# Kernel tuning notes

Hardware: AMD Instinct MI355X
Metric: run time of the kernel (lower is better)

## Reference

```python
import jax, jax.numpy as jnp
import numpy as np

B, N, D, H = 64, 257, 1024, 16
HD = D // H  # 64


def setup_inputs() -> dict:
    key = jax.random.key(0)
    k1, k2, k3, k4, k5, k6 = jax.random.split(key, 6)
    x = jax.random.normal(k1, (B, N, D), dtype=jnp.float32)
    # boolean key mask per batch; never mask CLS token (col 0) so no fully-masked rows
    mask = jax.random.randint(k2, (B, N), 0, 2) > 0
    mask = mask.at[:, 0].set(False)
    s = 1.0 / np.sqrt(D)
    in_proj_w = jax.random.normal(k3, (3 * D, D), dtype=jnp.float32) * s
    in_proj_b = jax.random.normal(k4, (3 * D,), dtype=jnp.float32) * 0.02
    out_proj_w = jax.random.normal(k5, (D, D), dtype=jnp.float32) * s
    out_proj_b = jax.random.normal(k6, (D,), dtype=jnp.float32) * 0.02
    return {"x": x, "mask": mask, "in_proj_w": in_proj_w, "in_proj_b": in_proj_b,
            "out_proj_w": out_proj_w, "out_proj_b": out_proj_b}


def reference(x, mask, in_proj_w, in_proj_b, out_proj_w, out_proj_b):
    b, n, d = x.shape
    h, hd = H, d // H
    # fused QKV projection: [b, n, 3*d]
    qkv = jnp.einsum('bnd,ed->bne', x, in_proj_w) + in_proj_b
    # einops 'b n (qkv h d) -> qkv b h n d'
    qkv = qkv.reshape(b, n, 3, h, hd).transpose(2, 0, 3, 1, 4)
    q, k, v = qkv[0], qkv[1], qkv[2]  # each [b, h, n, hd]
    attn_weights = jnp.einsum('bhqe,bhke->bhqk', q, k) / jnp.sqrt(jnp.asarray(hd, x.dtype))
    # mode == 'mask': -inf on masked keys (broadcast over heads and queries)
    attn_weights = jnp.where(mask[:, None, None, :], -jnp.inf, attn_weights)
    attn_matrix = jax.nn.softmax(attn_weights, axis=-1)
    out = jnp.einsum('bhqk,bhke->bhqe', attn_matrix, v)  # [b, h, n, hd]
    out = out.transpose(0, 2, 1, 3).reshape(b, n, d)      # 'b h n d -> b n (h d)'
    return jnp.einsum('bnd,ed->bne', out, out_proj_w) + out_proj_b
```

## Files before the change

### kernel.cpp

```cpp
#include <hip/hip_runtime.h>

#define B_   64
#define N_   257
#define D_   1024
#define H_   16
#define HD_  64
#define M_   (B_*N_)
#define CK_  96
#define VTS_ 128
#define PLS_ 104

typedef __bf16 bf16x8 __attribute__((ext_vector_type(8)));
typedef __bf16 bf16x4 __attribute__((ext_vector_type(4)));
typedef float  f32x4  __attribute__((ext_vector_type(4)));

__device__ __forceinline__ void gload_lds16(const void* g, void* l) {
    __builtin_amdgcn_global_load_lds(
        (const __attribute__((address_space(1))) void*)g,
        (__attribute__((address_space(3))) void*)l, 16, 0, 0);
}

#define MEMF() asm volatile("" ::: "memory")
#define BARRIER() do { MEMF(); __builtin_amdgcn_s_barrier(); MEMF(); } while (0)
#define WAITV(n) asm volatile("s_waitcnt vmcnt(" #n ")" ::: "memory")

#define XQ_  4210688
#define W1Q_ 786432
#define W2Q_ 262144
__global__ __launch_bounds__(256) void cvt_all(const float* __restrict__ x,
                                               const float* __restrict__ w1,
                                               const float* __restrict__ w2,
                                               __bf16* __restrict__ xb,
                                               __bf16* __restrict__ w1b,
                                               __bf16* __restrict__ w2b) {
    int i = blockIdx.x * 256 + threadIdx.x;
    const float* src; __bf16* dst; int j;
    if (i < XQ_) { src = x; dst = xb; j = i; }
    else if (i < XQ_ + W1Q_) { src = w1; dst = w1b; j = i - XQ_; }
    else if (i < XQ_ + W1Q_ + W2Q_) { src = w2; dst = w2b; j = i - XQ_ - W1Q_; }
    else return;
    float4 v = reinterpret_cast<const float4*>(src)[j];
    bf16x4 o;
    o[0] = (__bf16)v.x; o[1] = (__bf16)v.y; o[2] = (__bf16)v.z; o[3] = (__bf16)v.w;
    *reinterpret_cast<bf16x4*>(dst + (size_t)j * 4) = o;
}

template<int NT, int MODE>
__global__ __launch_bounds__(512, 2) void gemm256(const __bf16* __restrict__ A,
                                                  const __bf16* __restrict__ W,
                                                  const float* __restrict__ bias,
                                                  __bf16* __restrict__ qo,
                                                  __bf16* __restrict__ ko,
                                                  __bf16* __restrict__ vo,
                                                  float* __restrict__ fo) {
    __shared__ __align__(16) char smem[131072];
    constexpr int NWG = 65 * NT;
    constexpr int qd = NWG >> 3, rm = NWG & 7;
    const int orig = blockIdx.x;
    const int xcd = orig & 7, loc = orig >> 3;
    const int wgid = (xcd < rm ? xcd * (qd + 1) : rm * (qd + 1) + (xcd - rm) * qd) + loc;
    const int rowt = wgid / NT, colt = wgid - rowt * NT;
    const int row0 = rowt * 256, col0 = colt * 256;

    const int tid = threadIdx.x, lane = tid & 63, wv = tid >> 6;
    const int wm = wv >> 2, wn = wv & 3;
    const int fr = lane & 15, fq = lane >> 4, frs = lane & 7;

    const int pr = tid >> 3;
    const int pg = ((tid & 7) ^ (pr & 7)) * 8;
    int srcA[4];
    {
        const int prow[4] = {0, 128, 64, 192};
#pragma unroll
        for (int p = 0; p < 4; ++p) {
            int rg = row0 + prow[p] + pr;
            if (rg > M_ - 1) rg = M_ - 1;
            srcA[p] = rg * 1024 + pg;
        }
    }
    int srcW[2], ldsW[2];
#pragma unroll
    for (int e = 0; e < 2; ++e) {
        const int wb = (wv >> 1) * 64 + e * 16 + (wv & 1) * 8;
        srcW[e] = (col0 + wb + (lane >> 3)) * 1024 + pg;
        ldsW[e] = wb * 128;
    }
    char* const At0 = smem;
    char* const At1 = smem + 32768;
    char* const Wt0 = smem + 65536;
    char* const Wt1 = smem + 98304;

#define STG_AF(dst, kk) do { gload_lds16(A + srcA[0] + (kk), (dst) + wv * 1024); \
                             gload_lds16(A + srcA[1] + (kk), (dst) + 16384 + wv * 1024); } while (0)
#define STG_AB(dst, kk) do { gload_lds16(A + srcA[2] + (kk), (dst) + 8192 + wv * 1024); \
                             gload_lds16(A + srcA[3] + (kk), (dst) + 24576 + wv * 1024); } while (0)
#define STG_WF(dst, kk) do { gload_lds16(W + srcW[0] + (kk), (dst) + ldsW[0]); \
                             gload_lds16(W + srcW[1] + (kk), (dst) + ldsW[1]); } while (0)
#define STG_WB(dst, kk) do { gload_lds16(W + srcW[0] + 32768 + (kk), (dst) + ldsW[0] + 4096); \
                             gload_lds16(W + srcW[1] + 32768 + (kk), (dst) + ldsW[1] + 4096); } while (0)
#define LD_A(buf, rqo) do { \
    _Pragma("unroll") for (int i = 0; i < 4; ++i) \
    _Pragma("unroll") for (int ks = 0; ks < 2; ++ks) \
        af[i][ks] = *(const bf16x8*)((buf) + (wm * 128 + (rqo) + i * 16 + fr) * 128 \
                                           + (((ks * 4 + fq) ^ frs) << 4)); \
} while (0)
#define LD_B(buf, co, bw) do { \
    _Pragma("unroll") for (int j = 0; j < 2; ++j) \
    _Pragma("unroll") for (int ks = 0; ks < 2; ++ks) \
        bw[j][ks] = *(const bf16x8*)((buf) + (wn * 64 + (co) + j * 16 + fr) * 128 \
                                           + (((ks * 4 + fq) ^ frs) << 4)); \
} while (0)
#define MFMA_Q(i0, j0, bw) do { \
    __builtin_amdgcn_s_setprio(1); \
    _Pragma("unroll") for (int i = 0; i < 4; ++i) \
    _Pragma("unroll") for (int j = 0; j < 2; ++j) \
    _Pragma("unroll") for (int ks = 0; ks < 2; ++ks) \
        acc[(i0) + i][(j0) + j] = __builtin_amdgcn_mfma_f32_16x16x32_bf16( \
            af[i][ks], bw[j][ks], acc[(i0) + i][(j0) + j], 0, 0, 0); \
    __builtin_amdgcn_s_setprio(0); \
} while (0)

    f32x4 acc[8][4] = {};
    bf16x8 af[4][2], bw0[2][2], bw1[2][2];

    STG_AF(At0, 0); STG_WF(Wt0, 0); STG_WB(Wt0, 0); STG_AB(At0, 0);
    WAITV(4);
    BARRIER();

#pragma unroll 2
    for (int t = 0; t < 16; ++t) {
        char* const Ac = (t & 1) ? At1 : At0;
        char* const Wc = (t & 1) ? Wt1 : Wt0;
        char* const An = (t & 1) ? At0 : At1;
        char* const Wn = (t & 1) ? Wt0 : Wt1;
        const int kk = (t < 15) ? (t + 1) * 64 : 960;
        LD_A(Ac, 0);
        LD_B(Wc, 0, bw0);
        STG_AF(An, kk);
        WAITV(4);
        BARRIER();
        MFMA_Q(0, 0, bw0);
        BARRIER();
        LD_B(Wc, 32, bw1);
        STG_WF(Wn, kk);
        WAITV(4);
        BARRIER();
        MFMA_Q(0, 2, bw1);
        BARRIER();
        LD_A(Ac, 64);
        STG_WB(Wn, kk);
        BARRIER();
        MFMA_Q(4, 2, bw1);
        BARRIER();
        STG_AB(An, kk);
        WAITV(4);
        BARRIER();
        MFMA_Q(4, 0, bw0);
        BARRIER();
    }
    WAITV(0);
    BARRIER();

    if constexpr (MODE == 0) {
        const int which = colt >> 2;
        __bf16* const dst = which == 0 ? qo : (which == 1 ? ko : vo);
        const float scale = which == 0 ? 0.125f : 1.0f;
        float bj[4];
#pragma unroll
        for (int j = 0; j < 4; ++j) bj[j] = bias[col0 + wn * 64 + j * 16 + fr];
        __bf16* const Ct = (__bf16*)smem;
#pragma unroll
        for (int i = 0; i < 8; ++i) {
            const int rb = wm * 128 + (i >> 2) * 64 + (i & 3) * 16 + fq * 4;
#pragma unroll
            for (int r = 0; r < 4; ++r) {
                const int row = rb + r;
#pragma unroll
                for (int j = 0; j < 4; ++j) {
                    const int cu = wn * 64 + j * 16 + fr;
                    Ct[row * 256 + (((cu >> 3) ^ (row & 7)) * 8) + (cu & 7)] =
                        (__bf16)((acc[i][j][r] + bj[j]) * scale);
                }
            }
        }
        BARRIER();
#pragma unroll
        for (int p = 0; p < 16; ++p) {
            const int row = p * 16 + (tid >> 5);
            const int m = row0 + row;
            if (m < M_) {
                const int gl = tid & 31;
                bf16x8 v = *(const bf16x8*)(Ct + row * 256 + ((gl ^ (row & 7)) * 8));
                const int cG = col0 + gl * 8;
                const int h = (cG >> 6) & 15, hd = cG & 63;
                const int bb = m / 257, nn = m - bb * 257;
                *reinterpret_cast<bf16x8*>(dst + ((size_t)(bb * 16 + h) * 257 + nn) * 64 + hd) = v;
            }
        }
    } else {
        float bj[4];
#pragma unroll
        for (int j = 0; j < 4; ++j) bj[j] = bias[col0 + wn * 64 + j * 16 + fr];
#pragma unroll
        for (int i = 0; i < 8; ++i) {
            const int rb = wm * 128 + (i >> 2) * 64 + (i & 3) * 16 + fq * 4;
#pragma unroll
            for (int r = 0; r < 4; ++r) {
                const int m = row0 + rb + r;
                if (m < M_) {
                    float* const p = fo + (size_t)m * 1024 + col0 + wn * 64 + fr;
#pragma unroll
                    for (int j = 0; j < 4; ++j) p[j * 16] = acc[i][j][r] + bj[j];
                }
            }
        }
    }
#undef STG_AF
#undef STG_AB
#undef STG_WF
#undef STG_WB
#undef LD_A
#undef LD_B
#undef MFMA_Q
}

__global__ __launch_bounds__(256) void attn_kernel(const __bf16* __restrict__ qw,
                                                   const __bf16* __restrict__ kw,
                                                   const __bf16* __restrict__ vw,
                                                   const int* __restrict__ mask,
                                                   __bf16* __restrict__ attn) {
    const int bh = blockIdx.x;
    const int bb = bh >> 4, hh = bh & 15;
    const int q0 = blockIdx.y * 64;
    const int tid = threadIdx.x, lane = tid & 63, wv = tid >> 6;
    const int fr = lane & 15, fq = lane >> 4;
    const float NEG_INF = -__builtin_inff();

    __shared__ __align__(16) __bf16 Qs[64 * 64];
    __shared__ __align__(16) __bf16 Ks[CK_ * 64];
    __shared__ __align__(16) __bf16 Vt[64 * VTS_];
    __shared__ __align__(16) __bf16 Pl[4][16 * PLS_];
    __shared__ float maskb[288];

    const __bf16* qg = qw + ((size_t)bh * 257 + q0) * 64;
    const __bf16* kg = kw + (size_t)bh * 257 * 64;
    const __bf16* vg = vw + (size_t)bh * 257 * 64;
    const int* mg = mask + bb * 257;

    for (int idx = tid; idx < 288; idx += 256)
        maskb[idx] = (idx < 257 && mg[idx] == 0) ? 0.0f : NEG_INF;

#pragma unroll
    for (int i = 0; i < 2; ++i) {
        const int c = tid + i * 256;
        const int r = c >> 3, g = (c & 7) ^ (r & 7);
        gload_lds16(qg + (size_t)r * 64 + g * 8, (char*)Qs + i * 4096 + wv * 1024);
    }

    float m_run[4] = {NEG_INF, NEG_INF, NEG_INF, NEG_INF};
    float l_run[4] = {};
    f32x4 Oa[4] = {};

    for (int c3 = 0; c3 < 3; ++c3) {
        const int k0 = c3 * CK_;
        __syncthreads();
#pragma unroll
        for (int i = 0; i < 3; ++i) {
            const int c = tid + i * 256;
            const int r = c >> 3, g = (c & 7) ^ (r & 7);
            if (k0 + r < 257)
                gload_lds16(kg + (size_t)(k0 + r) * 64 + g * 8, (char*)Ks + i * 4096 + wv * 1024);
        }
#pragma unroll
        for (int it = 0; it < 3; ++it) {
            const int t = tid + it * 256;
            const int key = t >> 3, grp = t & 7;
            if (k0 + key < 257) {
                bf16x8 v8 = *reinterpret_cast<const bf16x8*>(vg + (size_t)(k0 + key) * 64 + grp * 8);
#pragma unroll
                for (int u = 0; u < 8; ++u) {
                    const int hd = grp * 8 + u;
                    Vt[hd * VTS_ + (((key >> 3) ^ (hd & 7)) * 8) + (key & 7)] = v8[u];
                }
            }
        }
        __syncthreads();

        f32x4 s[6];
        {
            bf16x8 aq[2];
#pragma unroll
            for (int ks = 0; ks < 2; ++ks)
                aq[ks] = *reinterpret_cast<const bf16x8*>(
                    &Qs[(wv * 16 + fr) * 64 + (((ks * 4 + fq) ^ (fr & 7)) * 8)]);
#pragma unroll
            for (int nt = 0; nt < 6; ++nt) {
                f32x4 sa = {};
#pragma unroll
                for (int ks = 0; ks < 2; ++ks) {
                    bf16x8 bk = *reinterpret_cast<const bf16x8*>(
                        &Ks[(nt * 16 + fr) * 64 + (((ks * 4 + fq) ^ (fr & 7)) * 8)]);
                    sa = __builtin_amdgcn_mfma_f32_16x16x32_bf16(aq[ks], bk, sa, 0, 0, 0);
                }
                const float mb = maskb[k0 + nt * 16 + fr];
#pragma unroll
                for (int r = 0; r < 4; ++r) sa[r] += mb;
                s[nt] = sa;
            }
        }
        float alpha[4];
#pragma unroll
        for (int r = 0; r < 4; ++r) {
            float v = s[0][r];
#pragma unroll
            for (int nt = 1; nt < 6; ++nt) v = fmaxf(v, s[nt][r]);
            v = fmaxf(v, __shfl_xor(v, 1));
            v = fmaxf(v, __shfl_xor(v, 2));
            v = fmaxf(v, __shfl_xor(v, 4));
            v = fmaxf(v, __shfl_xor(v, 8));
            const float mnew = fmaxf(m_run[r], v);
            alpha[r] = __expf(m_run[r] - mnew);
            m_run[r] = mnew;
        }
        float sm[4] = {};
#pragma unroll
        for (int nt = 0; nt < 6; ++nt)
#pragma unroll
            for (int r = 0; r < 4; ++r) {
                const float p = __expf(s[nt][r] - m_run[r]);
                s[nt][r] = p;
                sm[r] += p;
            }
#pragma unroll
        for (int r = 0; r < 4; ++r) {
            float v = sm[r];
            v += __shfl_xor(v, 1);
            v += __shfl_xor(v, 2);
            v += __shfl_xor(v, 4);
            v += __shfl_xor(v, 8);
            l_run[r] = l_run[r] * alpha[r] + v;
        }
#pragma unroll
        for (int ot = 0; ot < 4; ++ot)
#pragma unroll
            for (int r = 0; r < 4; ++r) Oa[ot][r] *= alpha[r];
#pragma unroll
        for (int nt = 0; nt < 6; ++nt)
#pragma unroll
            for (int r = 0; r < 4; ++r)
                Pl[wv][(fq * 4 + r) * PLS_ + nt * 16 + fr] = (__bf16)s[nt][r];
        __syncthreads();
        bf16x8 ap[3];
#pragma unroll
        for (int kk = 0; kk < 3; ++kk)
            ap[kk] = *reinterpret_cast<const bf16x8*>(&Pl[wv][fr * PLS_ + kk * 32 + fq * 8]);
#pragma unroll
        for (int ot = 0; ot < 4; ++ot) {
            const int row = ot * 16 + fr;
#pragma unroll
            for (int kk = 0; kk < 3; ++kk) {
                bf16x8 bv = *reinterpret_cast<const bf16x8*>(
                    &Vt[row * VTS_ + (((kk * 4 + fq) ^ (fr & 7)) * 8)]);
                Oa[ot] = __builtin_amdgcn_mfma_f32_16x16x32_bf16(ap[kk], bv, Oa[ot], 0, 0, 0);
            }
        }
    }
#pragma unroll
    for (int r = 0; r < 4; ++r) {
        const int n = q0 + wv * 16 + fq * 4 + r;
        const float inv = 1.0f / l_run[r];
#pragma unroll
        for (int ot = 0; ot < 4; ++ot)
            attn[((size_t)(bb * 257 + n)) * 1024 + hh * 64 + ot * 16 + fr] =
                (__bf16)(Oa[ot][r] * inv);
    }
}

__global__ __launch_bounds__(320) void attn_tail(const __bf16* __restrict__ qw,
                                                 const __bf16* __restrict__ kw,
                                                 const __bf16* __restrict__ vw,
                                                 const int* __restrict__ mask,
                                                 __bf16* __restrict__ attn) {
    const int bh = blockIdx.x;
    const int bb = bh >> 4, hh = bh & 15;
    const int tid = threadIdx.x, wv = tid >> 6;
    const float NEG_INF = -__builtin_inff();
    __shared__ float pbuf[257];
    __shared__ float red[5];
    __shared__ float gstat[2];

    const __bf16* qg = qw + ((size_t)bh * 257 + 256) * 64;
    const __bf16* kg = kw + (size_t)bh * 257 * 64;
    const __bf16* vg = vw + (size_t)bh * 257 * 64;

    float s = NEG_INF;
    if (tid < 257) {
        const __bf16* kr = kg + (size_t)tid * 64;
        float acc = 0.0f;
#pragma unroll
        for (int g = 0; g < 8; ++g) {
            bf16x8 qv = *reinterpret_cast<const bf16x8*>(qg + g * 8);
            bf16x8 kv = *reinterpret_cast<const bf16x8*>(kr + g * 8);
#pragma unroll
            for (int u = 0; u < 8; ++u) acc += (float)qv[u] * (float)kv[u];
        }
        s = (mask[bb * 257 + tid] == 0) ? acc : NEG_INF;
    }
    float v = s;
#pragma unroll
    for (int d = 1; d < 64; d <<= 1) v = fmaxf(v, __shfl_xor(v, d));
    if ((tid & 63) == 0) red[wv] = v;
    __syncthreads();
    if (tid == 0) {
        float m = red[0];
#pragma unroll
        for (int w = 1; w < 5; ++w) m = fmaxf(m, red[w]);
        gstat[0] = m;
    }
    __syncthreads();
    const float gmax = gstat[0];
    float p = (tid < 257) ? __expf(s - gmax) : 0.0f;
    if (tid < 257) pbuf[tid] = p;
    float sv = p;
#pragma unroll
    for (int d = 1; d < 64; d <<= 1) sv += __shfl_xor(sv, d);
    if ((tid & 63) == 0) red[wv] = sv;
    __syncthreads();
    if (tid == 0) gstat[1] = red[0] + red[1] + red[2] + red[3] + red[4];
    __syncthreads();
    if (tid < 64) {
        const float inv = 1.0f / gstat[1];
        float o = 0.0f;
        for (int j = 0; j < 257; ++j)
            o += pbuf[j] * (float)vg[(size_t)j * 64 + tid];
        attn[((size_t)(bb * 257 + 256)) * 1024 + hh * 64 + tid] = (__bf16)(o * inv);
    }
}

extern "C" void kernel_launch(void* const* d_in, const int* in_sizes, int n_in,
                              void* d_out, int out_size, void* d_ws, size_t ws_size,
                              hipStream_t stream) {
    const float* x  = (const float*)d_in[0];
    const int* mask = (const int*)d_in[1];
    const float* w1 = (const float*)d_in[2];
    const float* b1 = (const float*)d_in[3];
    const float* w2 = (const float*)d_in[4];
    const float* b2 = (const float*)d_in[5];
    float* out = (float*)d_out;
    char* ws = (char*)d_ws;
    __bf16* x_bf  = (__bf16*)(ws);
    __bf16* w1_bf = (__bf16*)(ws + 33816576);
    __bf16* w2_bf = (__bf16*)(ws + 40108032);
    __bf16* q_ws  = (__bf16*)(ws + 42205184);
    __bf16* k_ws  = (__bf16*)(ws + 75890688);
    __bf16* v_ws  = (__bf16*)(ws + 109576192);
    __bf16* a_bf  = (__bf16*)(ws + 143261696);

    cvt_all<<<20544, 256, 0, stream>>>(x, w1, w2, x_bf, w1_bf, w2_bf);
    gemm256<12, 0><<<780, 512, 0, stream>>>(x_bf, w1_bf, b1, q_ws, k_ws, v_ws, nullptr);
    attn_kernel<<<dim3(1024, 4), 256, 0, stream>>>(q_ws, k_ws, v_ws, mask, a_bf);
    attn_tail<<<1024, 320, 0, stream>>>(q_ws, k_ws, v_ws, mask, a_bf);
    gemm256<4, 1><<<260, 512, 0, stream>>>(a_bf, w2_bf, b2, nullptr, nullptr, nullptr, out);
}
```

Baseline: 428.7 us.

## Split GEMM ragged row tail into separate small kernel and deepen prefetch

The main 256x256 GEMMs now cover only the 16384 full rows (64 row tiles), which drops the row clamping and bounds checks and simplifies the XCD work mapping. The last 64 rows go to a new small gemm_tail kernel with 64x128 tiles. The K-loop also issues all four next-tile global-to-LDS loads at the top of each iteration with adjusted waitcnt values, to overlap them better with compute. In exchange there is an extra kernel launch and a poorly utilised tail kernel of 24 or 8 blocks.

```diff
diff --git a/kernel.cpp b/kernel.cpp
--- a/kernel.cpp
+++ b/kernel.cpp
@@ -54,11 +54,11 @@
                                                   __bf16* __restrict__ vo,
                                                   float* __restrict__ fo) {
     __shared__ __align__(16) char smem[131072];
-    constexpr int NWG = 65 * NT;
-    constexpr int qd = NWG >> 3, rm = NWG & 7;
+    constexpr int NWG = 64 * NT;
+    constexpr int qd = NWG >> 3;
     const int orig = blockIdx.x;
     const int xcd = orig & 7, loc = orig >> 3;
-    const int wgid = (xcd < rm ? xcd * (qd + 1) : rm * (qd + 1) + (xcd - rm) * qd) + loc;
+    const int wgid = xcd * qd + loc;
     const int rowt = wgid / NT, colt = wgid - rowt * NT;
     const int row0 = rowt * 256, col0 = colt * 256;
 
@@ -73,8 +73,7 @@
         const int prow[4] = {0, 128, 64, 192};
 #pragma unroll
         for (int p = 0; p < 4; ++p) {
-            int rg = row0 + prow[p] + pr;
-            if (rg > M_ - 1) rg = M_ - 1;
+            const int rg = row0 + prow[p] + pr;
             srcA[p] = rg * 1024 + pg;
         }
     }
@@ -137,22 +136,22 @@
         LD_A(Ac, 0);
         LD_B(Wc, 0, bw0);
         STG_AF(An, kk);
-        WAITV(4);
+        STG_WF(Wn, kk);
+        STG_WB(Wn, kk);
+        STG_AB(An, kk);
+        WAITV(10);
         BARRIER();
         MFMA_Q(0, 0, bw0);
         BARRIER();
         LD_B(Wc, 32, bw1);
-        STG_WF(Wn, kk);
-        WAITV(4);
+        WAITV(8);
         BARRIER();
         MFMA_Q(0, 2, bw1);
         BARRIER();
         LD_A(Ac, 64);
-        STG_WB(Wn, kk);
         BARRIER();
         MFMA_Q(4, 2, bw1);
         BARRIER();
-        STG_AB(An, kk);
         WAITV(4);
         BARRIER();
         MFMA_Q(4, 0, bw0);
@@ -188,14 +187,12 @@
         for (int p = 0; p < 16; ++p) {
             const int row = p * 16 + (tid >> 5);
             const int m = row0 + row;
-            if (m < M_) {
-                const int gl = tid & 31;
-                bf16x8 v = *(const bf16x8*)(Ct + row * 256 + ((gl ^ (row & 7)) * 8));
-                const int cG = col0 + gl * 8;
-                const int h = (cG >> 6) & 15, hd = cG & 63;
-                const int bb = m / 257, nn = m - bb * 257;
-                *reinterpret_cast<bf16x8*>(dst + ((size_t)(bb * 16 + h) * 257 + nn) * 64 + hd) = v;
-            }
+            const int gl = tid & 31;
+            bf16x8 v = *(const bf16x8*)(Ct + row * 256 + ((gl ^ (row & 7)) * 8));
+            const int cG = col0 + gl * 8;
+            const int h = (cG >> 6) & 15, hd = cG & 63;
+            const int bb = m / 257, nn = m - bb * 257;
+            *reinterpret_cast<bf16x8*>(dst + ((size_t)(bb * 16 + h) * 257 + nn) * 64 + hd) = v;
         }
     } else {
         float bj[4];
@@ -207,11 +204,9 @@
 #pragma unroll
             for (int r = 0; r < 4; ++r) {
                 const int m = row0 + rb + r;
-                if (m < M_) {
-                    float* const p = fo + (size_t)m * 1024 + col0 + wn * 64 + fr;
-#pragma unroll
-                    for (int j = 0; j < 4; ++j) p[j * 16] = acc[i][j][r] + bj[j];
-                }
+                float* const p = fo + (size_t)m * 1024 + col0 + wn * 64 + fr;
+#pragma unroll
+                for (int j = 0; j < 4; ++j) p[j * 16] = acc[i][j][r] + bj[j];
             }
         }
     }
@@ -222,6 +217,78 @@
 #undef LD_A
 #undef LD_B
 #undef MFMA_Q
+}
+
+template<int MODE>
+__global__ __launch_bounds__(256) void gemm_tail(const __bf16* __restrict__ A,
+                                                 const __bf16* __restrict__ W,
+                                                 const float* __restrict__ bias,
+                                                 __bf16* __restrict__ qo,
+                                                 __bf16* __restrict__ ko,
+                                                 __bf16* __restrict__ vo,
+                                                 float* __restrict__ fo) {
+    __shared__ __align__(16) __bf16 As[64 * 64];
+    __shared__ __align__(16) __bf16 Ws[128 * 64];
+    const int col0 = blockIdx.x * 128;
+    const int tid = threadIdx.x, lane = tid & 63, wv = tid >> 6;
+    const int fr = lane & 15, fq = lane >> 4, frs = lane & 7;
+
+    f32x4 acc[4][2] = {};
+    for (int k0 = 0; k0 < 1024; k0 += 64) {
+        __syncthreads();
+#pragma unroll
+        for (int i = 0; i < 2; ++i) {
+            const int c = tid + i * 256;
+            const int r = c >> 3, g = (c & 7) ^ (r & 7);
+            gload_lds16(A + (size_t)(16384 + r) * 1024 + g * 8 + k0,
+                        (char*)As + i * 4096 + wv * 1024);
+        }
+#pragma unroll
+        for (int i = 0; i < 4; ++i) {
+            const int c = tid + i * 256;
+            const int r = c >> 3, g = (c & 7) ^ (r & 7);
+            gload_lds16(W + (size_t)(col0 + r) * 1024 + g * 8 + k0,
+                        (char*)Ws + i * 4096 + wv * 1024);
+        }
+        __syncthreads();
+#pragma unroll
+        for (int ks = 0; ks < 2; ++ks) {
+            const int goff = ((ks * 4 + fq) ^ frs) * 8;
+            bf16x8 af[4], bw[2];
+#pragma unroll
+            for (int i = 0; i < 4; ++i)
+                af[i] = *reinterpret_cast<const bf16x8*>(&As[(i * 16 + fr) * 64 + goff]);
+#pragma unroll
+            for (int j = 0; j < 2; ++j)
+                bw[j] = *reinterpret_cast<const bf16x8*>(&Ws[(wv * 32 + j * 16 + fr) * 64 + goff]);
+#pragma unroll
+            for (int i = 0; i < 4; ++i)
+#pragma unroll
+                for (int j = 0; j < 2; ++j)
+                    acc[i][j] = __builtin_amdgcn_mfma_f32_16x16x32_bf16(af[i], bw[j], acc[i][j], 0, 0, 0);
+        }
+    }
+#pragma unroll
+    for (int i = 0; i < 4; ++i)
+#pragma unroll
+        for (int r = 0; r < 4; ++r) {
+            const int rowC = i * 16 + fq * 4 + r;
+            const int nn = 193 + rowC;
+#pragma unroll
+            for (int j = 0; j < 2; ++j) {
+                const int cG = col0 + wv * 32 + j * 16 + fr;
+                if constexpr (MODE == 0) {
+                    const int which = cG >> 10;
+                    __bf16* const dst = which == 0 ? qo : (which == 1 ? ko : vo);
+                    const float scale = which == 0 ? 0.125f : 1.0f;
+                    const int h = (cG >> 6) & 15, hd = cG & 63;
+                    dst[((size_t)(63 * 16 + h) * 257 + nn) * 64 + hd] =
+                        (__bf16)((acc[i][j][r] + bias[cG]) * scale);
+                } else {
+                    fo[(size_t)(16384 + rowC) * 1024 + cG] = acc[i][j][r] + bias[cG];
+                }
+            }
+        }
 }
 
 __global__ __launch_bounds__(256) void attn_kernel(const __bf16* __restrict__ qw,
@@ -457,8 +524,10 @@
     __bf16* a_bf  = (__bf16*)(ws + 143261696);
 
     cvt_all<<<20544, 256, 0, stream>>>(x, w1, w2, x_bf, w1_bf, w2_bf);
-    gemm256<12, 0><<<780, 512, 0, stream>>>(x_bf, w1_bf, b1, q_ws, k_ws, v_ws, nullptr);
+    gemm256<12, 0><<<768, 512, 0, stream>>>(x_bf, w1_bf, b1, q_ws, k_ws, v_ws, nullptr);
+    gemm_tail<0><<<24, 256, 0, stream>>>(x_bf, w1_bf, b1, q_ws, k_ws, v_ws, nullptr);
     attn_kernel<<<dim3(1024, 4), 256, 0, stream>>>(q_ws, k_ws, v_ws, mask, a_bf);
     attn_tail<<<1024, 320, 0, stream>>>(q_ws, k_ws, v_ws, mask, a_bf);
-    gemm256<4, 1><<<260, 512, 0, stream>>>(a_bf, w2_bf, b2, nullptr, nullptr, nullptr, out);
-}
+    gemm256<4, 1><<<256, 512, 0, stream>>>(a_bf, w2_bf, b2, nullptr, nullptr, nullptr, out);
+    gemm_tail<1><<<8, 256, 0, stream>>>(a_bf, w2_bf, b2, nullptr, nullptr, nullptr, out);
+}
```

New measurement: 416.8 us. 2.8% less time.
